# Optimization experiments

Hardware: AMD Instinct MI355X
Metric: run time of the kernel (lower is better)

The kernel has to match this reference:

```python
import jax, jax.numpy as jnp
import numpy as np

N, E, U, EF, STEPS = 5000, 40000, 64, 16, 4


def setup_inputs() -> dict:
    key = jax.random.key(0)
    ks = jax.random.split(key, 7)
    node_features = jax.random.normal(ks[0], (N, U), dtype=jnp.float32)
    edge_features = jax.random.normal(ks[1], (E, EF), dtype=jnp.float32)
    pair_indices = jax.random.randint(ks[2], (E, 2), 0, N, dtype=jnp.int32)
    # EdgeNetwork params: kernel (efc, nfc*nfc), bias (nfc*nfc,)
    edge_kernel = jax.random.normal(ks[3], (EF, U * U), dtype=jnp.float32) * 0.05
    edge_bias = jnp.zeros((U * U,), dtype=jnp.float32)
    # Keras GRUCell (reset_after=True): kernel (in, 3u), recurrent (u, 3u), bias (2, 3u)
    gru_kernel = jax.random.normal(ks[4], (U, 3 * U), dtype=jnp.float32) * 0.05
    gru_recurrent_kernel = jax.random.normal(ks[5], (U, 3 * U), dtype=jnp.float32) * 0.05
    gru_bias = jnp.zeros((2, 3 * U), dtype=jnp.float32)
    return {
        "node_features": node_features,
        "edge_features": edge_features,
        "pair_indices": pair_indices,
        "edge_kernel": edge_kernel,
        "edge_bias": edge_bias,
        "gru_kernel": gru_kernel,
        "gru_recurrent_kernel": gru_recurrent_kernel,
        "gru_bias": gru_bias,
    }


def _gru_cell(x, h, kernel, rkernel, bias):
    # Keras GRUCell math with reset_after=True
    u = h.shape[-1]
    mx = x @ kernel + bias[0]          # [N, 3u]
    mh = h @ rkernel + bias[1]         # [N, 3u]
    xz, xr, xh = mx[:, :u], mx[:, u:2 * u], mx[:, 2 * u:]
    iz, ir, ih = mh[:, :u], mh[:, u:2 * u], mh[:, 2 * u:]
    z = jax.nn.sigmoid(xz + iz)
    r = jax.nn.sigmoid(xr + ir)
    hh = jnp.tanh(xh + r * ih)
    return z * h + (1.0 - z) * hh


def reference(node_features, edge_features, pair_indices, edge_kernel, edge_bias,
              gru_kernel, gru_recurrent_kernel, gru_bias):
    n = node_features.shape[0]
    u = node_features.shape[1]  # units (pad_length = 0 since nfc == units)
    src = pair_indices[:, 0]
    nbr = pair_indices[:, 1]
    # Edge matrices are loop-invariant: [E, u, u]
    edge_mats = (edge_features @ edge_kernel + edge_bias).reshape(-1, u, u)
    h = node_features
    for _ in range(STEPS):
        nb = h[nbr]                                    # gather [E, u]
        msg = jnp.einsum('eij,ej->ei', edge_mats, nb)  # per-edge matvec
        agg = jax.ops.segment_sum(msg, src, num_segments=n)  # scatter-sum [N, u]
        h = _gru_cell(agg, h, gru_kernel, gru_recurrent_kernel, gru_bias)
    return h
```

## Files before the change

kernel.cpp:

```cpp
#include <hip/hip_runtime.h>
#include <math.h>

#define NN 5000
#define NE 40000
#define UU 64
#define FE 16
#define FEP 17
#define KD (FEP*UU)
#define LDK (KD+8)
#define NSTEPS 4
#define NT 8
#define NB (NN/NT)
#define SLOT 40
#define CH 8
#define WBN (UU*KD)
#define GTN (192*64)

typedef _Float16 half8 __attribute__((ext_vector_type(8)));
typedef float f32x4 __attribute__((ext_vector_type(4)));

__device__ __forceinline__ float sigm(float x){ return 1.f/(1.f + __expf(-x)); }
__device__ __forceinline__ int rfl(int x){ return __builtin_amdgcn_readfirstlane(x); }

__global__ void build_k(const float* __restrict__ ek, const float* __restrict__ eb,
                        const float* __restrict__ gk, const float* __restrict__ rk,
                        _Float16* __restrict__ wb, _Float16* __restrict__ gkt,
                        _Float16* __restrict__ rkt, int* __restrict__ deg){
  int tid = blockIdx.x*blockDim.x + threadIdx.x;
  if (tid < NN) deg[tid] = 0;
  if (tid < WBN){
    int i = tid / KD, k = tid - i*KD;
    int f = k >> 6, j = k & 63;
    float v = (f < FE) ? ek[f*4096 + i*64 + j] : eb[i*64 + j];
    wb[tid] = (_Float16)v;
  } else if (tid < WBN + GTN){
    int r = tid - WBN; int n = r >> 6, k = r & 63;
    gkt[r] = (_Float16)gk[k*192 + n];
  } else if (tid < WBN + 2*GTN){
    int r = tid - WBN - GTN; int n = r >> 6, k = r & 63;
    rkt[r] = (_Float16)rk[k*192 + n];
  }
}

__global__ void bucket_k(const int* __restrict__ pair, int* __restrict__ deg,
                         int* __restrict__ eidb){
  int e = blockIdx.x*blockDim.x + threadIdx.x;
  if (e < NE){
    int v = pair[2*e];
    int pos = atomicAdd(&deg[v], 1);
    if (pos < SLOT) eidb[v*SLOT + pos] = e;
  }
}

__global__ __launch_bounds__(512) void prep_k(const int* __restrict__ pair,
                       const int* __restrict__ deg,
                       const int* __restrict__ eidb, int2* __restrict__ enb){
  int w = threadIdx.x >> 6, lane = threadIdx.x & 63;
  int v = blockIdx.x * 8 + w;
  if (v >= NN) return;
  int dg = deg[v]; if (dg > SLOT) dg = SLOT;
  if (lane < dg){
    int e = eidb[v*SLOT + lane];
    int rank = 0;
    for (int j=0; j<dg; ++j){ int ej = eidb[v*SLOT + j]; rank += (ej < e); }
    enb[v*SLOT + rank] = make_int2(e, pair[2*e + 1]);
  }
}

__global__ __launch_bounds__(512) void step_k(const float* __restrict__ h_in,
        float* __restrict__ h_out, const float* __restrict__ ef,
        const int* __restrict__ deg, const int2* __restrict__ enb,
        const _Float16* __restrict__ wb, const _Float16* __restrict__ gkt,
        const _Float16* __restrict__ rkt, const float* __restrict__ gb){
  __shared__ _Float16 Gs[NT*LDK];
  __shared__ _Float16 aggT[NT*72];
  __shared__ _Float16 hT[NT*72];

  int tid = threadIdx.x;
  int w = tid >> 6, lane = tid & 63;
  int r16 = lane & 15, kh = lane >> 4;
  int vb = blockIdx.x * NT;
  int v  = vb + w;

  hT[w*72 + lane] = (_Float16)h_in[(size_t)v*64 + lane];

  {
    int dgv = rfl(deg[v]); if (dgv > SLOT) dgv = SLOT;
    const int2* lst = enb + v*SLOT;
    float g[FEP];
    #pragma unroll
    for (int f=0;f<FEP;++f) g[f] = 0.f;
    for (int c0=0; c0<dgv; c0+=CH){
      int ee[CH], nb[CH];
      #pragma unroll
      for (int q=0;q<CH;++q){ int i=c0+q;
        if (i<dgv){ int2 p = lst[i]; ee[q]=rfl(p.x); nb[q]=rfl(p.y); }
        else { ee[q]=0; nb[q]=0; } }
      float hj[CH];
      #pragma unroll
      for (int q=0;q<CH;++q){ int i=c0+q;
        hj[q] = (i<dgv) ? h_in[(size_t)nb[q]*64 + lane] : 0.f; }
      #pragma unroll
      for (int q=0;q<CH;++q){ int i=c0+q;
        if (i<dgv){
          const float4* er = (const float4*)(ef + (size_t)ee[q]*FE);
          float4 e0 = er[0], e1 = er[1], e2 = er[2], e3 = er[3];
          g[ 0]=fmaf(e0.x,hj[q],g[ 0]); g[ 1]=fmaf(e0.y,hj[q],g[ 1]);
          g[ 2]=fmaf(e0.z,hj[q],g[ 2]); g[ 3]=fmaf(e0.w,hj[q],g[ 3]);
          g[ 4]=fmaf(e1.x,hj[q],g[ 4]); g[ 5]=fmaf(e1.y,hj[q],g[ 5]);
          g[ 6]=fmaf(e1.z,hj[q],g[ 6]); g[ 7]=fmaf(e1.w,hj[q],g[ 7]);
          g[ 8]=fmaf(e2.x,hj[q],g[ 8]); g[ 9]=fmaf(e2.y,hj[q],g[ 9]);
          g[10]=fmaf(e2.z,hj[q],g[10]); g[11]=fmaf(e2.w,hj[q],g[11]);
          g[12]=fmaf(e3.x,hj[q],g[12]); g[13]=fmaf(e3.y,hj[q],g[13]);
          g[14]=fmaf(e3.z,hj[q],g[14]); g[15]=fmaf(e3.w,hj[q],g[15]);
          g[16] += hj[q];
        } }
    }
    #pragma unroll
    for (int f=0;f<FEP;++f) Gs[w*LDK + f*64 + lane] = (_Float16)g[f];
  }
  __syncthreads();

  if (w < 4){
    f32x4 acc = {0.f,0.f,0.f,0.f};
    const _Float16* ap = Gs + (r16 & 7)*LDK + kh*8;
    const _Float16* bp = wb + (size_t)(w*16 + r16)*KD + kh*8;
    #pragma unroll 4
    for (int k0=0; k0<KD; k0+=32){
      half8 a = *(const half8*)(ap + k0);
      half8 b = *(const half8*)(bp + k0);
      acc = __builtin_amdgcn_mfma_f32_16x16x32_f16(a, b, acc, 0, 0, 0);
    }
    if (kh < 2){
      #pragma unroll
      for (int r=0;r<4;++r) aggT[(kh*4+r)*72 + w*16 + r16] = (_Float16)acc[r];
    }
  }
  __syncthreads();

  if (w < 4){
    int uw = w*16 + r16;
    const _Float16* az = aggT + (r16 & 7)*72 + kh*8;
    const _Float16* ah = hT   + (r16 & 7)*72 + kh*8;
    f32x4 mxz={0.f,0.f,0.f,0.f}, mxr=mxz, mxh=mxz, mhz=mxz, mhr=mxz, mhh=mxz;
    #pragma unroll
    for (int ks=0; ks<2; ++ks){
      half8 aa = *(const half8*)(az + ks*32);
      half8 hh = *(const half8*)(ah + ks*32);
      half8 bz = *(const half8*)(gkt + (size_t)(      uw)*64 + ks*32 + kh*8);
      half8 br = *(const half8*)(gkt + (size_t)( 64 + uw)*64 + ks*32 + kh*8);
      half8 bh = *(const half8*)(gkt + (size_t)(128 + uw)*64 + ks*32 + kh*8);
      half8 cz = *(const half8*)(rkt + (size_t)(      uw)*64 + ks*32 + kh*8);
      half8 cr = *(const half8*)(rkt + (size_t)( 64 + uw)*64 + ks*32 + kh*8);
      half8 ch = *(const half8*)(rkt + (size_t)(128 + uw)*64 + ks*32 + kh*8);
      mxz = __builtin_amdgcn_mfma_f32_16x16x32_f16(aa, bz, mxz, 0,0,0);
      mxr = __builtin_amdgcn_mfma_f32_16x16x32_f16(aa, br, mxr, 0,0,0);
      mxh = __builtin_amdgcn_mfma_f32_16x16x32_f16(aa, bh, mxh, 0,0,0);
      mhz = __builtin_amdgcn_mfma_f32_16x16x32_f16(hh, cz, mhz, 0,0,0);
      mhr = __builtin_amdgcn_mfma_f32_16x16x32_f16(hh, cr, mhr, 0,0,0);
      mhh = __builtin_amdgcn_mfma_f32_16x16x32_f16(hh, ch, mhh, 0,0,0);
    }
    if (kh < 2){
      float b0z = gb[uw],      b0r = gb[64+uw],  b0h = gb[128+uw];
      float b1z = gb[192+uw],  b1r = gb[256+uw], b1h = gb[320+uw];
      #pragma unroll
      for (int r=0;r<4;++r){
        int row = vb + kh*4 + r;
        float z  = sigm(mxz[r] + b0z + mhz[r] + b1z);
        float rr = sigm(mxr[r] + b0r + mhr[r] + b1r);
        float hc = tanhf(mxh[r] + b0h + rr*(mhh[r] + b1h));
        float hold = h_in[(size_t)row*64 + uw];
        h_out[(size_t)row*64 + uw] = z*hold + (1.f - z)*hc;
      }
    }
  }
}

extern "C" void kernel_launch(void* const* d_in, const int* in_sizes, int n_in,
                              void* d_out, int out_size, void* d_ws, size_t ws_size,
                              hipStream_t stream){
  const float* nodef = (const float*)d_in[0];
  const float* edgef = (const float*)d_in[1];
  const int*   pair  = (const int*)  d_in[2];
  const float* ek    = (const float*)d_in[3];
  const float* ebias = (const float*)d_in[4];
  const float* gk    = (const float*)d_in[5];
  const float* rk    = (const float*)d_in[6];
  const float* gb    = (const float*)d_in[7];

  char* ws = (char*)d_ws;
  size_t o = 0;
  auto carve = [&](size_t bytes)->char*{
    char* p = ws + o; o = (o + bytes + 255) & ~255ULL; return p; };
  int*      deg  = (int*)     carve(NN*sizeof(int));
  int*      eidb = (int*)     carve((size_t)NN*SLOT*sizeof(int));
  int2*     enb  = (int2*)    carve((size_t)NN*SLOT*sizeof(int2));
  _Float16* wb   = (_Float16*)carve((size_t)WBN*sizeof(_Float16));
  _Float16* gkt  = (_Float16*)carve((size_t)GTN*sizeof(_Float16));
  _Float16* rkt  = (_Float16*)carve((size_t)GTN*sizeof(_Float16));
  float*    hA   = (float*)   carve((size_t)NN*UU*sizeof(float));
  float*    hB   = (float*)   carve((size_t)NN*UU*sizeof(float));

  build_k <<<(WBN+2*GTN+255)/256, 256, 0, stream>>>(ek, ebias, gk, rk, wb, gkt, rkt, deg);
  bucket_k<<<(NE+255)/256, 256, 0, stream>>>(pair, deg, eidb);
  prep_k  <<<NB, 512, 0, stream>>>(pair, deg, eidb, enb);

  const float* hin = nodef;
  for (int s=0; s<NSTEPS; ++s){
    float* hout = (s == NSTEPS-1) ? (float*)d_out : ((s & 1) ? hB : hA);
    step_k<<<NB, 512, 0, stream>>>(hin, hout, edgef, deg, enb,
                                   wb, gkt, rkt, gb);
    hin = hout;
  }
}
```

Baseline: 114.9 us.

## Split GRU work across idle waves and prefetch edge weights before gather

Waves 0-3 now load the first eight edge-weight fragments into registers before the neighbour gather, so those loads overlap the gather latency. Waves 4-7, previously idle during the edge matmul, compute the recurrent h-projection and load the GRU input weights in parallel with it. After the barrier they run the input projection and the gate epilogue. The launch bound of 512 threads with a minimum of 4 blocks limits register use, and the prefetched fragments raise register pressure, so spilling is possible.

Result: slower. 132.5 us (+15.3%).

```diff
diff --git a/kernel.cpp b/kernel.cpp
--- a/kernel.cpp
+++ b/kernel.cpp
@@ -13,6 +13,7 @@
 #define NB (NN/NT)
 #define SLOT 40
 #define CH 8
+#define NPRE 8
 #define WBN (UU*KD)
 #define GTN (192*64)
 
@@ -67,7 +68,7 @@
   }
 }
 
-__global__ __launch_bounds__(512) void step_k(const float* __restrict__ h_in,
+__global__ __launch_bounds__(512, 4) void step_k(const float* __restrict__ h_in,
         float* __restrict__ h_out, const float* __restrict__ ef,
         const int* __restrict__ deg, const int2* __restrict__ enb,
         const _Float16* __restrict__ wb, const _Float16* __restrict__ gkt,
@@ -81,6 +82,25 @@
   int r16 = lane & 15, kh = lane >> 4;
   int vb = blockIdx.x * NT;
   int v  = vb + w;
+  int uw2 = (w & 3)*16 + r16;
+
+  half8 bpre[NPRE];
+  half8 wz0,wz1,wr0,wr1,wh0,wh1;
+  float b0z,b0r,b0h,b1z,b1r,b1h;
+  if (w < 4){
+    const _Float16* bp = wb + (size_t)(w*16 + r16)*KD + kh*8;
+    #pragma unroll
+    for (int i=0;i<NPRE;++i) bpre[i] = *(const half8*)(bp + i*32);
+  } else {
+    const _Float16* rz = rkt + (size_t)(      uw2)*64 + kh*8;
+    const _Float16* rr = rkt + (size_t)( 64 + uw2)*64 + kh*8;
+    const _Float16* rh = rkt + (size_t)(128 + uw2)*64 + kh*8;
+    wz0 = *(const half8*)(rz); wz1 = *(const half8*)(rz + 32);
+    wr0 = *(const half8*)(rr); wr1 = *(const half8*)(rr + 32);
+    wh0 = *(const half8*)(rh); wh1 = *(const half8*)(rh + 32);
+    b0z = gb[uw2];     b0r = gb[64+uw2];  b0h = gb[128+uw2];
+    b1z = gb[192+uw2]; b1r = gb[256+uw2]; b1h = gb[320+uw2];
+  }
 
   hT[w*72 + lane] = (_Float16)h_in[(size_t)v*64 + lane];
 
@@ -121,12 +141,20 @@
   }
   __syncthreads();
 
+  f32x4 mhz={0.f,0.f,0.f,0.f}, mhr=mhz, mhh=mhz;
+  half8 gz0,gz1,gr0,gr1,gh0,gh1;
+
   if (w < 4){
     f32x4 acc = {0.f,0.f,0.f,0.f};
     const _Float16* ap = Gs + (r16 & 7)*LDK + kh*8;
     const _Float16* bp = wb + (size_t)(w*16 + r16)*KD + kh*8;
+    #pragma unroll
+    for (int i=0;i<NPRE;++i){
+      half8 a = *(const half8*)(ap + i*32);
+      acc = __builtin_amdgcn_mfma_f32_16x16x32_f16(a, bpre[i], acc, 0, 0, 0);
+    }
     #pragma unroll 4
-    for (int k0=0; k0<KD; k0+=32){
+    for (int k0=NPRE*32; k0<KD; k0+=32){
       half8 a = *(const half8*)(ap + k0);
       half8 b = *(const half8*)(bp + k0);
       acc = __builtin_amdgcn_mfma_f32_16x16x32_f16(a, b, acc, 0, 0, 0);
@@ -135,42 +163,45 @@
       #pragma unroll
       for (int r=0;r<4;++r) aggT[(kh*4+r)*72 + w*16 + r16] = (_Float16)acc[r];
     }
+  } else {
+    const _Float16* ah = hT + (r16 & 7)*72 + kh*8;
+    half8 h0 = *(const half8*)(ah);
+    half8 h1 = *(const half8*)(ah + 32);
+    mhz = __builtin_amdgcn_mfma_f32_16x16x32_f16(h0, wz0, mhz, 0,0,0);
+    mhz = __builtin_amdgcn_mfma_f32_16x16x32_f16(h1, wz1, mhz, 0,0,0);
+    mhr = __builtin_amdgcn_mfma_f32_16x16x32_f16(h0, wr0, mhr, 0,0,0);
+    mhr = __builtin_amdgcn_mfma_f32_16x16x32_f16(h1, wr1, mhr, 0,0,0);
+    mhh = __builtin_amdgcn_mfma_f32_16x16x32_f16(h0, wh0, mhh, 0,0,0);
+    mhh = __builtin_amdgcn_mfma_f32_16x16x32_f16(h1, wh1, mhh, 0,0,0);
+    const _Float16* gz = gkt + (size_t)(      uw2)*64 + kh*8;
+    const _Float16* gr = gkt + (size_t)( 64 + uw2)*64 + kh*8;
+    const _Float16* gh = gkt + (size_t)(128 + uw2)*64 + kh*8;
+    gz0 = *(const half8*)(gz); gz1 = *(const half8*)(gz + 32);
+    gr0 = *(const half8*)(gr); gr1 = *(const half8*)(gr + 32);
+    gh0 = *(const half8*)(gh); gh1 = *(const half8*)(gh + 32);
   }
   __syncthreads();
 
-  if (w < 4){
-    int uw = w*16 + r16;
+  if (w >= 4){
     const _Float16* az = aggT + (r16 & 7)*72 + kh*8;
-    const _Float16* ah = hT   + (r16 & 7)*72 + kh*8;
-    f32x4 mxz={0.f,0.f,0.f,0.f}, mxr=mxz, mxh=mxz, mhz=mxz, mhr=mxz, mhh=mxz;
-    #pragma unroll
-    for (int ks=0; ks<2; ++ks){
-      half8 aa = *(const half8*)(az + ks*32);
-      half8 hh = *(const half8*)(ah + ks*32);
-      half8 bz = *(const half8*)(gkt + (size_t)(      uw)*64 + ks*32 + kh*8);
-      half8 br = *(const half8*)(gkt + (size_t)( 64 + uw)*64 + ks*32 + kh*8);
-      half8 bh = *(const half8*)(gkt + (size_t)(128 + uw)*64 + ks*32 + kh*8);
-      half8 cz = *(const half8*)(rkt + (size_t)(      uw)*64 + ks*32 + kh*8);
-      half8 cr = *(const half8*)(rkt + (size_t)( 64 + uw)*64 + ks*32 + kh*8);
-      half8 ch = *(const half8*)(rkt + (size_t)(128 + uw)*64 + ks*32 + kh*8);
-      mxz = __builtin_amdgcn_mfma_f32_16x16x32_f16(aa, bz, mxz, 0,0,0);
-      mxr = __builtin_amdgcn_mfma_f32_16x16x32_f16(aa, br, mxr, 0,0,0);
-      mxh = __builtin_amdgcn_mfma_f32_16x16x32_f16(aa, bh, mxh, 0,0,0);
-      mhz = __builtin_amdgcn_mfma_f32_16x16x32_f16(hh, cz, mhz, 0,0,0);
-      mhr = __builtin_amdgcn_mfma_f32_16x16x32_f16(hh, cr, mhr, 0,0,0);
-      mhh = __builtin_amdgcn_mfma_f32_16x16x32_f16(hh, ch, mhh, 0,0,0);
-    }
+    half8 a0 = *(const half8*)(az);
+    half8 a1 = *(const half8*)(az + 32);
+    f32x4 mxz={0.f,0.f,0.f,0.f}, mxr=mxz, mxh=mxz;
+    mxz = __builtin_amdgcn_mfma_f32_16x16x32_f16(a0, gz0, mxz, 0,0,0);
+    mxz = __builtin_amdgcn_mfma_f32_16x16x32_f16(a1, gz1, mxz, 0,0,0);
+    mxr = __builtin_amdgcn_mfma_f32_16x16x32_f16(a0, gr0, mxr, 0,0,0);
+    mxr = __builtin_amdgcn_mfma_f32_16x16x32_f16(a1, gr1, mxr, 0,0,0);
+    mxh = __builtin_amdgcn_mfma_f32_16x16x32_f16(a0, gh0, mxh, 0,0,0);
+    mxh = __builtin_amdgcn_mfma_f32_16x16x32_f16(a1, gh1, mxh, 0,0,0);
     if (kh < 2){
-      float b0z = gb[uw],      b0r = gb[64+uw],  b0h = gb[128+uw];
-      float b1z = gb[192+uw],  b1r = gb[256+uw], b1h = gb[320+uw];
       #pragma unroll
       for (int r=0;r<4;++r){
         int row = vb + kh*4 + r;
         float z  = sigm(mxz[r] + b0z + mhz[r] + b1z);
         float rr = sigm(mxr[r] + b0r + mhr[r] + b1r);
         float hc = tanhf(mxh[r] + b0h + rr*(mhh[r] + b1h));
-        float hold = h_in[(size_t)row*64 + uw];
-        h_out[(size_t)row*64 + uw] = z*hold + (1.f - z)*hc;
+        float hold = h_in[(size_t)row*64 + uw2];
+        h_out[(size_t)row*64 + uw2] = z*hold + (1.f - z)*hc;
       }
     }
   }
```

## Process 16 nodes per block with split-K edge-matrix MFMA across all waves

Applied to the files above, without the earlier changes.

Each block now handles 16 nodes instead of 8. Each wave gathers neighbour features for two nodes at once, so all 16 rows of the MFMA tile are filled instead of 8. The per-node edge-matrix product is split along K across all 8 waves, with fp32 partial sums reduced through shared memory. This halves the block count and doubles the reuse of each edge-kernel weight load. In exchange it adds a barrier and reduction pass, higher register pressure from two accumulator sets, and load imbalance when the two nodes in a wave have different degrees.

Result: no change. 116.0 us (+1.0%).

```diff
diff --git a/kernel.cpp b/kernel.cpp
--- a/kernel.cpp
+++ b/kernel.cpp
@@ -7,10 +7,11 @@
 #define FE 16
 #define FEP 17
 #define KD (FEP*UU)
+#define KH2 (KD/2)
 #define LDK (KD+8)
 #define NSTEPS 4
-#define NT 8
-#define NB (NN/NT)
+#define NT 16
+#define NB ((NN+NT-1)/NT)
 #define SLOT 40
 #define CH 8
 #define WBN (UU*KD)
@@ -73,75 +74,109 @@
         const _Float16* __restrict__ wb, const _Float16* __restrict__ gkt,
         const _Float16* __restrict__ rkt, const float* __restrict__ gb){
   __shared__ _Float16 Gs[NT*LDK];
-  __shared__ _Float16 aggT[NT*72];
-  __shared__ _Float16 hT[NT*72];
+  __shared__ float    aggP[2][16][68];
+  __shared__ _Float16 aggT[16*72];
+  __shared__ _Float16 hT[16*72];
 
   int tid = threadIdx.x;
   int w = tid >> 6, lane = tid & 63;
   int r16 = lane & 15, kh = lane >> 4;
   int vb = blockIdx.x * NT;
-  int v  = vb + w;
-
-  hT[w*72 + lane] = (_Float16)h_in[(size_t)v*64 + lane];
+
+  for (int i=tid; i<NT*64; i+=512){
+    int lv = i >> 6, j = i & 63; int v = vb + lv;
+    hT[lv*72 + j] = (_Float16)((v < NN) ? h_in[(size_t)v*64 + j] : 0.f);
+  }
 
   {
-    int dgv = rfl(deg[v]); if (dgv > SLOT) dgv = SLOT;
-    const int2* lst = enb + v*SLOT;
-    float g[FEP];
-    #pragma unroll
-    for (int f=0;f<FEP;++f) g[f] = 0.f;
-    for (int c0=0; c0<dgv; c0+=CH){
-      int ee[CH], nb[CH];
+    int v0 = vb + w*2, v1 = v0 + 1;
+    int d0 = (v0 < NN) ? deg[v0] : 0; if (d0 > SLOT) d0 = SLOT; d0 = rfl(d0);
+    int d1 = (v1 < NN) ? deg[v1] : 0; if (d1 > SLOT) d1 = SLOT; d1 = rfl(d1);
+    const int2* l0 = enb + (size_t)v0*SLOT;
+    const int2* l1 = enb + (size_t)v1*SLOT;
+    float gA[FEP], gB[FEP];
+    #pragma unroll
+    for (int f=0;f<FEP;++f){ gA[f] = 0.f; gB[f] = 0.f; }
+    int dmax = (d0 > d1) ? d0 : d1;
+    for (int c0=0; c0<dmax; c0+=CH){
+      int eA[CH], nA[CH], eB[CH], nB[CH];
       #pragma unroll
       for (int q=0;q<CH;++q){ int i=c0+q;
-        if (i<dgv){ int2 p = lst[i]; ee[q]=rfl(p.x); nb[q]=rfl(p.y); }
-        else { ee[q]=0; nb[q]=0; } }
-      float hj[CH];
+        if (i<d0){ int2 p = l0[i]; eA[q]=rfl(p.x); nA[q]=rfl(p.y); }
+        else { eA[q]=0; nA[q]=0; }
+        if (i<d1){ int2 p = l1[i]; eB[q]=rfl(p.x); nB[q]=rfl(p.y); }
+        else { eB[q]=0; nB[q]=0; } }
+      float hA[CH], hB[CH];
       #pragma unroll
       for (int q=0;q<CH;++q){ int i=c0+q;
-        hj[q] = (i<dgv) ? h_in[(size_t)nb[q]*64 + lane] : 0.f; }
+        hA[q] = (i<d0) ? h_in[(size_t)nA[q]*64 + lane] : 0.f;
+        hB[q] = (i<d1) ? h_in[(size_t)nB[q]*64 + lane] : 0.f; }
       #pragma unroll
       for (int q=0;q<CH;++q){ int i=c0+q;
-        if (i<dgv){
-          const float4* er = (const float4*)(ef + (size_t)ee[q]*FE);
+        if (i<d0){
+          const float4* er = (const float4*)(ef + (size_t)eA[q]*FE);
           float4 e0 = er[0], e1 = er[1], e2 = er[2], e3 = er[3];
-          g[ 0]=fmaf(e0.x,hj[q],g[ 0]); g[ 1]=fmaf(e0.y,hj[q],g[ 1]);
-          g[ 2]=fmaf(e0.z,hj[q],g[ 2]); g[ 3]=fmaf(e0.w,hj[q],g[ 3]);
-          g[ 4]=fmaf(e1.x,hj[q],g[ 4]); g[ 5]=fmaf(e1.y,hj[q],g[ 5]);
-          g[ 6]=fmaf(e1.z,hj[q],g[ 6]); g[ 7]=fmaf(e1.w,hj[q],g[ 7]);
-          g[ 8]=fmaf(e2.x,hj[q],g[ 8]); g[ 9]=fmaf(e2.y,hj[q],g[ 9]);
-          g[10]=fmaf(e2.z,hj[q],g[10]); g[11]=fmaf(e2.w,hj[q],g[11]);
-          g[12]=fmaf(e3.x,hj[q],g[12]); g[13]=fmaf(e3.y,hj[q],g[13]);
-          g[14]=fmaf(e3.z,hj[q],g[14]); g[15]=fmaf(e3.w,hj[q],g[15]);
-          g[16] += hj[q];
+          float hj = hA[q];
+          gA[ 0]=fmaf(e0.x,hj,gA[ 0]); gA[ 1]=fmaf(e0.y,hj,gA[ 1]);
+          gA[ 2]=fmaf(e0.z,hj,gA[ 2]); gA[ 3]=fmaf(e0.w,hj,gA[ 3]);
+          gA[ 4]=fmaf(e1.x,hj,gA[ 4]); gA[ 5]=fmaf(e1.y,hj,gA[ 5]);
+          gA[ 6]=fmaf(e1.z,hj,gA[ 6]); gA[ 7]=fmaf(e1.w,hj,gA[ 7]);
+          gA[ 8]=fmaf(e2.x,hj,gA[ 8]); gA[ 9]=fmaf(e2.y,hj,gA[ 9]);
+          gA[10]=fmaf(e2.z,hj,gA[10]); gA[11]=fmaf(e2.w,hj,gA[11]);
+          gA[12]=fmaf(e3.x,hj,gA[12]); gA[13]=fmaf(e3.y,hj,gA[13]);
+          gA[14]=fmaf(e3.z,hj,gA[14]); gA[15]=fmaf(e3.w,hj,gA[15]);
+          gA[16] += hj;
+        }
+        if (i<d1){
+          const float4* er = (const float4*)(ef + (size_t)eB[q]*FE);
+          float4 e0 = er[0], e1 = er[1], e2 = er[2], e3 = er[3];
+          float hj = hB[q];
+          gB[ 0]=fmaf(e0.x,hj,gB[ 0]); gB[ 1]=fmaf(e0.y,hj,gB[ 1]);
+          gB[ 2]=fmaf(e0.z,hj,gB[ 2]); gB[ 3]=fmaf(e0.w,hj,gB[ 3]);
+          gB[ 4]=fmaf(e1.x,hj,gB[ 4]); gB[ 5]=fmaf(e1.y,hj,gB[ 5]);
+          gB[ 6]=fmaf(e1.z,hj,gB[ 6]); gB[ 7]=fmaf(e1.w,hj,gB[ 7]);
+          gB[ 8]=fmaf(e2.x,hj,gB[ 8]); gB[ 9]=fmaf(e2.y,hj,gB[ 9]);
+          gB[10]=fmaf(e2.z,hj,gB[10]); gB[11]=fmaf(e2.w,hj,gB[11]);
+          gB[12]=fmaf(e3.x,hj,gB[12]); gB[13]=fmaf(e3.y,hj,gB[13]);
+          gB[14]=fmaf(e3.z,hj,gB[14]); gB[15]=fmaf(e3.w,hj,gB[15]);
+          gB[16] += hj;
         } }
     }
     #pragma unroll
-    for (int f=0;f<FEP;++f) Gs[w*LDK + f*64 + lane] = (_Float16)g[f];
+    for (int f=0;f<FEP;++f){
+      Gs[(w*2  )*LDK + f*64 + lane] = (_Float16)gA[f];
+      Gs[(w*2+1)*LDK + f*64 + lane] = (_Float16)gB[f];
+    }
   }
   __syncthreads();
 
-  if (w < 4){
+  {
+    int cg = w & 3, khalf = w >> 2;
+    int koff = khalf * KH2;
     f32x4 acc = {0.f,0.f,0.f,0.f};
-    const _Float16* ap = Gs + (r16 & 7)*LDK + kh*8;
-    const _Float16* bp = wb + (size_t)(w*16 + r16)*KD + kh*8;
+    const _Float16* ap = Gs + r16*LDK + koff + kh*8;
+    const _Float16* bp = wb + (size_t)(cg*16 + r16)*KD + koff + kh*8;
     #pragma unroll 4
-    for (int k0=0; k0<KD; k0+=32){
+    for (int k0=0; k0<KH2; k0+=32){
       half8 a = *(const half8*)(ap + k0);
       half8 b = *(const half8*)(bp + k0);
       acc = __builtin_amdgcn_mfma_f32_16x16x32_f16(a, b, acc, 0, 0, 0);
     }
-    if (kh < 2){
-      #pragma unroll
-      for (int r=0;r<4;++r) aggT[(kh*4+r)*72 + w*16 + r16] = (_Float16)acc[r];
-    }
+    #pragma unroll
+    for (int r=0;r<4;++r) aggP[khalf][kh*4+r][cg*16 + r16] = acc[r];
+  }
+  __syncthreads();
+
+  for (int i=tid; i<NT*64; i+=512){
+    int rw = i >> 6, cl = i & 63;
+    aggT[rw*72 + cl] = (_Float16)(aggP[0][rw][cl] + aggP[1][rw][cl]);
   }
   __syncthreads();
 
   if (w < 4){
     int uw = w*16 + r16;
-    const _Float16* az = aggT + (r16 & 7)*72 + kh*8;
-    const _Float16* ah = hT   + (r16 & 7)*72 + kh*8;
+    const _Float16* az = aggT + r16*72 + kh*8;
+    const _Float16* ah = hT   + r16*72 + kh*8;
     f32x4 mxz={0.f,0.f,0.f,0.f}, mxr=mxz, mxh=mxz, mhz=mxz, mhr=mxz, mhh=mxz;
     #pragma unroll
     for (int ks=0; ks<2; ++ks){
@@ -160,12 +195,12 @@
       mhr = __builtin_amdgcn_mfma_f32_16x16x32_f16(hh, cr, mhr, 0,0,0);
       mhh = __builtin_amdgcn_mfma_f32_16x16x32_f16(hh, ch, mhh, 0,0,0);
     }
-    if (kh < 2){
-      float b0z = gb[uw],      b0r = gb[64+uw],  b0h = gb[128+uw];
-      float b1z = gb[192+uw],  b1r = gb[256+uw], b1h = gb[320+uw];
-      #pragma unroll
-      for (int r=0;r<4;++r){
-        int row = vb + kh*4 + r;
+    float b0z = gb[uw],      b0r = gb[64+uw],  b0h = gb[128+uw];
+    float b1z = gb[192+uw],  b1r = gb[256+uw], b1h = gb[320+uw];
+    #pragma unroll
+    for (int r=0;r<4;++r){
+      int row = vb + kh*4 + r;
+      if (row < NN){
         float z  = sigm(mxz[r] + b0z + mhz[r] + b1z);
         float rr = sigm(mxr[r] + b0r + mhr[r] + b1r);
         float hc = tanhf(mxh[r] + b0h + rr*(mhh[r] + b1h));
@@ -203,7 +238,7 @@
 
   build_k <<<(WBN+2*GTN+255)/256, 256, 0, stream>>>(ek, ebias, gk, rk, wb, gkt, rkt, deg);
   bucket_k<<<(NE+255)/256, 256, 0, stream>>>(pair, deg, eidb);
-  prep_k  <<<NB, 512, 0, stream>>>(pair, deg, eidb, enb);
+  prep_k  <<<(NN+7)/8, 512, 0, stream>>>(pair, deg, eidb, enb);
 
   const float* hin = nodef;
   for (int s=0; s<NSTEPS; ++s){
```

## Fuse preprocessing into one kernel, pack edge features per node, store hidden in fp16

Applied to the files above, without the earlier changes.

Replaces the three preprocessing kernels with one pack kernel. Each block buckets edges for a range of nodes in shared-memory atomics, then writes neighbour ids and a per-node contiguous copy of the edge features. The step kernel reads those packed features directly, spreads neighbour ids by lane shuffle, and keeps intermediate hidden states in fp16. The aim is fewer launches and less scattered gather traffic per step. The cost is extra packed storage, each pack block scanning all edges, and some precision loss in the intermediate states.

Result: slower. 132.5 us (+15.3%).

```diff
diff --git a/kernel.cpp b/kernel.cpp
--- a/kernel.cpp
+++ b/kernel.cpp
@@ -10,11 +10,13 @@
 #define LDK (KD+8)
 #define NSTEPS 4
 #define NT 8
-#define NB (NN/NT)
+#define NBS (NN/NT)
 #define SLOT 40
 #define CH 8
 #define WBN (UU*KD)
 #define GTN (192*64)
+#define PBLK 64
+#define NPB 79
 
 typedef _Float16 half8 __attribute__((ext_vector_type(8)));
 typedef float f32x4 __attribute__((ext_vector_type(4)));
@@ -22,54 +24,66 @@
 __device__ __forceinline__ float sigm(float x){ return 1.f/(1.f + __expf(-x)); }
 __device__ __forceinline__ int rfl(int x){ return __builtin_amdgcn_readfirstlane(x); }
 
-__global__ void build_k(const float* __restrict__ ek, const float* __restrict__ eb,
-                        const float* __restrict__ gk, const float* __restrict__ rk,
-                        _Float16* __restrict__ wb, _Float16* __restrict__ gkt,
-                        _Float16* __restrict__ rkt, int* __restrict__ deg){
-  int tid = blockIdx.x*blockDim.x + threadIdx.x;
-  if (tid < NN) deg[tid] = 0;
-  if (tid < WBN){
-    int i = tid / KD, k = tid - i*KD;
-    int f = k >> 6, j = k & 63;
-    float v = (f < FE) ? ek[f*4096 + i*64 + j] : eb[i*64 + j];
-    wb[tid] = (_Float16)v;
-  } else if (tid < WBN + GTN){
-    int r = tid - WBN; int n = r >> 6, k = r & 63;
-    gkt[r] = (_Float16)gk[k*192 + n];
-  } else if (tid < WBN + 2*GTN){
-    int r = tid - WBN - GTN; int n = r >> 6, k = r & 63;
-    rkt[r] = (_Float16)rk[k*192 + n];
+__global__ __launch_bounds__(1024) void pack_k(
+        const int* __restrict__ pair, const float* __restrict__ edgef,
+        const float* __restrict__ ek, const float* __restrict__ eb,
+        const float* __restrict__ gk, const float* __restrict__ rk,
+        _Float16* __restrict__ wb, _Float16* __restrict__ gkt,
+        _Float16* __restrict__ rkt,
+        int* __restrict__ deg, int* __restrict__ nbrP, float* __restrict__ efP){
+  __shared__ int cnt[NPB];
+  __shared__ int el[NPB*SLOT];
+
+  int t = threadIdx.x;
+  for (int gt = blockIdx.x*1024 + t; gt < WBN + 2*GTN; gt += PBLK*1024){
+    if (gt < WBN){
+      int i = gt / KD, k = gt - i*KD;
+      int f = k >> 6, j = k & 63;
+      float v = (f < FE) ? ek[f*4096 + i*64 + j] : eb[i*64 + j];
+      wb[gt] = (_Float16)v;
+    } else if (gt < WBN + GTN){
+      int r = gt - WBN; int n = r >> 6, k = r & 63;
+      gkt[r] = (_Float16)gk[k*192 + n];
+    } else {
+      int r = gt - WBN - GTN; int n = r >> 6, k = r & 63;
+      rkt[r] = (_Float16)rk[k*192 + n];
+    }
+  }
+
+  int lo = blockIdx.x * NPB;
+  int hi = lo + NPB; if (hi > NN) hi = NN;
+  for (int i=t; i<NPB; i+=1024) cnt[i] = 0;
+  __syncthreads();
+  for (int e=t; e<NE; e+=1024){
+    int2 pr = *(const int2*)(pair + 2*e);
+    if (pr.x >= lo && pr.x < hi){
+      int p = atomicAdd(&cnt[pr.x - lo], 1);
+      if (p < SLOT) el[(pr.x - lo)*SLOT + p] = e;
+    }
+  }
+  __syncthreads();
+  int w = t >> 6, lane = t & 63;
+  for (int n = w; n < hi - lo; n += 16){
+    int dg = cnt[n]; if (dg > SLOT) dg = SLOT;
+    int v = lo + n;
+    if (lane == 0) deg[v] = dg;
+    if (lane < dg){
+      int e = el[n*SLOT + lane];
+      int rank = 0;
+      for (int j=0; j<dg; ++j) rank += (el[n*SLOT + j] < e);
+      nbrP[(size_t)v*SLOT + rank] = pair[2*e + 1];
+      const float4* er = (const float4*)(edgef + (size_t)e*FE);
+      float4* ew = (float4*)(efP + ((size_t)v*SLOT + rank)*FE);
+      ew[0] = er[0]; ew[1] = er[1]; ew[2] = er[2]; ew[3] = er[3];
+    }
   }
 }
 
-__global__ void bucket_k(const int* __restrict__ pair, int* __restrict__ deg,
-                         int* __restrict__ eidb){
-  int e = blockIdx.x*blockDim.x + threadIdx.x;
-  if (e < NE){
-    int v = pair[2*e];
-    int pos = atomicAdd(&deg[v], 1);
-    if (pos < SLOT) eidb[v*SLOT + pos] = e;
-  }
-}
-
-__global__ __launch_bounds__(512) void prep_k(const int* __restrict__ pair,
-                       const int* __restrict__ deg,
-                       const int* __restrict__ eidb, int2* __restrict__ enb){
-  int w = threadIdx.x >> 6, lane = threadIdx.x & 63;
-  int v = blockIdx.x * 8 + w;
-  if (v >= NN) return;
-  int dg = deg[v]; if (dg > SLOT) dg = SLOT;
-  if (lane < dg){
-    int e = eidb[v*SLOT + lane];
-    int rank = 0;
-    for (int j=0; j<dg; ++j){ int ej = eidb[v*SLOT + j]; rank += (ej < e); }
-    enb[v*SLOT + rank] = make_int2(e, pair[2*e + 1]);
-  }
-}
-
-__global__ __launch_bounds__(512) void step_k(const float* __restrict__ h_in,
-        float* __restrict__ h_out, const float* __restrict__ ef,
-        const int* __restrict__ deg, const int2* __restrict__ enb,
+template<typename TIN, typename TOUT>
+__global__ __launch_bounds__(512) void step_k(const TIN* __restrict__ h_in,
+        TOUT* __restrict__ h_out,
+        const int* __restrict__ deg, const int* __restrict__ nbrP,
+        const float* __restrict__ efP,
         const _Float16* __restrict__ wb, const _Float16* __restrict__ gkt,
         const _Float16* __restrict__ rkt, const float* __restrict__ gb){
   __shared__ _Float16 Gs[NT*LDK];
@@ -82,38 +96,36 @@
   int vb = blockIdx.x * NT;
   int v  = vb + w;
 
-  hT[w*72 + lane] = (_Float16)h_in[(size_t)v*64 + lane];
+  hT[w*72 + lane] = (_Float16)(float)h_in[(size_t)v*64 + lane];
 
   {
-    int dgv = rfl(deg[v]); if (dgv > SLOT) dgv = SLOT;
-    const int2* lst = enb + v*SLOT;
+    int dg = deg[v]; if (dg > SLOT) dg = SLOT; dg = rfl(dg);
+    int nbr = (lane < dg) ? nbrP[(size_t)v*SLOT + lane] : 0;
+    const float* ebase = efP + (size_t)v*SLOT*FE;
     float g[FEP];
     #pragma unroll
     for (int f=0;f<FEP;++f) g[f] = 0.f;
-    for (int c0=0; c0<dgv; c0+=CH){
-      int ee[CH], nb[CH];
+    for (int c0=0; c0<dg; c0+=CH){
+      float hj[CH];
       #pragma unroll
       for (int q=0;q<CH;++q){ int i=c0+q;
-        if (i<dgv){ int2 p = lst[i]; ee[q]=rfl(p.x); nb[q]=rfl(p.y); }
-        else { ee[q]=0; nb[q]=0; } }
-      float hj[CH];
+        int nb = __shfl(nbr, i);
+        hj[q] = (i<dg) ? (float)h_in[(size_t)nb*64 + lane] : 0.f; }
       #pragma unroll
       for (int q=0;q<CH;++q){ int i=c0+q;
-        hj[q] = (i<dgv) ? h_in[(size_t)nb[q]*64 + lane] : 0.f; }
-      #pragma unroll
-      for (int q=0;q<CH;++q){ int i=c0+q;
-        if (i<dgv){
-          const float4* er = (const float4*)(ef + (size_t)ee[q]*FE);
+        if (i<dg){
+          const float4* er = (const float4*)(ebase + (size_t)i*FE);
           float4 e0 = er[0], e1 = er[1], e2 = er[2], e3 = er[3];
-          g[ 0]=fmaf(e0.x,hj[q],g[ 0]); g[ 1]=fmaf(e0.y,hj[q],g[ 1]);
-          g[ 2]=fmaf(e0.z,hj[q],g[ 2]); g[ 3]=fmaf(e0.w,hj[q],g[ 3]);
-          g[ 4]=fmaf(e1.x,hj[q],g[ 4]); g[ 5]=fmaf(e1.y,hj[q],g[ 5]);
-          g[ 6]=fmaf(e1.z,hj[q],g[ 6]); g[ 7]=fmaf(e1.w,hj[q],g[ 7]);
-          g[ 8]=fmaf(e2.x,hj[q],g[ 8]); g[ 9]=fmaf(e2.y,hj[q],g[ 9]);
-          g[10]=fmaf(e2.z,hj[q],g[10]); g[11]=fmaf(e2.w,hj[q],g[11]);
-          g[12]=fmaf(e3.x,hj[q],g[12]); g[13]=fmaf(e3.y,hj[q],g[13]);
-          g[14]=fmaf(e3.z,hj[q],g[14]); g[15]=fmaf(e3.w,hj[q],g[15]);
-          g[16] += hj[q];
+          float hj_ = hj[q];
+          g[ 0]=fmaf(e0.x,hj_,g[ 0]); g[ 1]=fmaf(e0.y,hj_,g[ 1]);
+          g[ 2]=fmaf(e0.z,hj_,g[ 2]); g[ 3]=fmaf(e0.w,hj_,g[ 3]);
+          g[ 4]=fmaf(e1.x,hj_,g[ 4]); g[ 5]=fmaf(e1.y,hj_,g[ 5]);
+          g[ 6]=fmaf(e1.z,hj_,g[ 6]); g[ 7]=fmaf(e1.w,hj_,g[ 7]);
+          g[ 8]=fmaf(e2.x,hj_,g[ 8]); g[ 9]=fmaf(e2.y,hj_,g[ 9]);
+          g[10]=fmaf(e2.z,hj_,g[10]); g[11]=fmaf(e2.w,hj_,g[11]);
+          g[12]=fmaf(e3.x,hj_,g[12]); g[13]=fmaf(e3.y,hj_,g[13]);
+          g[14]=fmaf(e3.z,hj_,g[14]); g[15]=fmaf(e3.w,hj_,g[15]);
+          g[16] += hj_;
         } }
     }
     #pragma unroll
@@ -169,8 +181,8 @@
         float z  = sigm(mxz[r] + b0z + mhz[r] + b1z);
         float rr = sigm(mxr[r] + b0r + mhr[r] + b1r);
         float hc = tanhf(mxh[r] + b0h + rr*(mhh[r] + b1h));
-        float hold = h_in[(size_t)row*64 + uw];
-        h_out[(size_t)row*64 + uw] = z*hold + (1.f - z)*hc;
+        float hold = (float)h_in[(size_t)row*64 + uw];
+        h_out[(size_t)row*64 + uw] = (TOUT)(z*hold + (1.f - z)*hc);
       }
     }
   }
@@ -193,23 +205,23 @@
   auto carve = [&](size_t bytes)->char*{
     char* p = ws + o; o = (o + bytes + 255) & ~255ULL; return p; };
   int*      deg  = (int*)     carve(NN*sizeof(int));
-  int*      eidb = (int*)     carve((size_t)NN*SLOT*sizeof(int));
-  int2*     enb  = (int2*)    carve((size_t)NN*SLOT*sizeof(int2));
+  int*      nbrP = (int*)     carve((size_t)NN*SLOT*sizeof(int));
+  float*    efP  = (float*)   carve((size_t)NN*SLOT*FE*sizeof(float));
   _Float16* wb   = (_Float16*)carve((size_t)WBN*sizeof(_Float16));
   _Float16* gkt  = (_Float16*)carve((size_t)GTN*sizeof(_Float16));
   _Float16* rkt  = (_Float16*)carve((size_t)GTN*sizeof(_Float16));
-  float*    hA   = (float*)   carve((size_t)NN*UU*sizeof(float));
-  float*    hB   = (float*)   carve((size_t)NN*UU*sizeof(float));
-
-  build_k <<<(WBN+2*GTN+255)/256, 256, 0, stream>>>(ek, ebias, gk, rk, wb, gkt, rkt, deg);
-  bucket_k<<<(NE+255)/256, 256, 0, stream>>>(pair, deg, eidb);
-  prep_k  <<<NB, 512, 0, stream>>>(pair, deg, eidb, enb);
-
-  const float* hin = nodef;
-  for (int s=0; s<NSTEPS; ++s){
-    float* hout = (s == NSTEPS-1) ? (float*)d_out : ((s & 1) ? hB : hA);
-    step_k<<<NB, 512, 0, stream>>>(hin, hout, edgef, deg, enb,
-                                   wb, gkt, rkt, gb);
-    hin = hout;
-  }
+  _Float16* h16A = (_Float16*)carve((size_t)NN*UU*sizeof(_Float16));
+  _Float16* h16B = (_Float16*)carve((size_t)NN*UU*sizeof(_Float16));
+
+  pack_k<<<PBLK, 1024, 0, stream>>>(pair, edgef, ek, ebias, gk, rk,
+                                    wb, gkt, rkt, deg, nbrP, efP);
+
+  step_k<float, _Float16><<<NBS, 512, 0, stream>>>(nodef, h16A, deg, nbrP, efP,
+                                                   wb, gkt, rkt, gb);
+  step_k<_Float16, _Float16><<<NBS, 512, 0, stream>>>(h16A, h16B, deg, nbrP, efP,
+                                                      wb, gkt, rkt, gb);
+  step_k<_Float16, _Float16><<<NBS, 512, 0, stream>>>(h16B, h16A, deg, nbrP, efP,
+                                                      wb, gkt, rkt, gb);
+  step_k<_Float16, float><<<NBS, 512, 0, stream>>>(h16A, (float*)d_out, deg, nbrP, efP,
+                                                   wb, gkt, rkt, gb);
 }
```
